# Performance work log

Hardware: AMD Instinct MI355X
Metric: run time of the kernel (lower is better)

Reference implementation:

```python
import jax, jax.numpy as jnp
import numpy as np

N_NODES = 50000
N_EDGES = 800000
IN_CH, HID_CH, OUT_CH = 128, 128, 64


def setup_inputs() -> dict:
    key = jax.random.key(0)
    k1, k2, k3, k4 = jax.random.split(key, 4)
    x = jax.random.normal(k1, (N_NODES, IN_CH), dtype=jnp.float32)
    edge_index = jax.random.randint(k2, (2, N_EDGES), 0, N_NODES, dtype=jnp.int64)
    # Glorot-style scaled weights (as in PyG GCNConv default init)
    W1 = jax.random.normal(k3, (IN_CH, HID_CH), dtype=jnp.float32) * (1.0 / np.sqrt(IN_CH))
    b1 = jnp.zeros((HID_CH,), dtype=jnp.float32)
    W2 = jax.random.normal(k4, (HID_CH, OUT_CH), dtype=jnp.float32) * (1.0 / np.sqrt(HID_CH))
    b2 = jnp.zeros((OUT_CH,), dtype=jnp.float32)
    return {"x": x, "edge_index": edge_index, "W1": W1, "b1": b1, "W2": W2, "b2": b2}


def _gcn_conv(x, src, dst, norm, W, b, n_nodes):
    # linear transform, then normalized gather-scatter aggregation
    h = x @ W                                   # [N, C_out]
    msgs = h[src] * norm[:, None]               # [E+N, C_out]
    agg = jax.ops.segment_sum(msgs, dst, num_segments=n_nodes)
    return agg + b


def reference(x, edge_index, W1, b1, W2, b2):
    n = x.shape[0]
    # add self-loops (PyG GCNConv default)
    loops = jnp.arange(n, dtype=edge_index.dtype)
    src = jnp.concatenate([edge_index[0], loops])  # message source (x_j)
    dst = jnp.concatenate([edge_index[1], loops])  # aggregation target
    # symmetric normalization: deg computed over targets incl. self-loops
    deg = jax.ops.segment_sum(jnp.ones_like(dst, dtype=x.dtype), dst, num_segments=n)
    dinv = jnp.where(deg > 0, jax.lax.rsqrt(deg), 0.0)
    norm = dinv[src] * dinv[dst]                # [E+N]

    h = _gcn_conv(x, src, dst, norm, W1, b1, n)
    h = jax.nn.relu(h)
    out = _gcn_conv(h, src, dst, norm, W2, b2, n)
    return out
```

## Files before the change

### kernel.cpp

```cpp
#include <hip/hip_runtime.h>
#include <hip/hip_bf16.h>


#define NPB 196
#define NBMAX 1024
#define CAP 4096

using short8 = __attribute__((ext_vector_type(8))) short;
using f32x4  = __attribute__((ext_vector_type(4))) float;

__device__ __forceinline__ unsigned short f2bf(float f) {
    unsigned int u = __float_as_uint(f);
    unsigned int r = u + 0x7fffu + ((u >> 16) & 1u);
    return (unsigned short)(r >> 16);
}

__global__ void k_zerob(int* __restrict__ p, int n) {
    int i = blockIdx.x * blockDim.x + threadIdx.x;
    if (i < n) p[i] = 0;
}

__global__ __launch_bounds__(256) void k_bhist(const int* __restrict__ dst,
                                               int* __restrict__ bhist,
                                               int nb, int e) {
    __shared__ int hist[NBMAX];
    const int tid = threadIdx.x;
    for (int b = tid; b < nb; b += 256) hist[b] = 0;
    __syncthreads();
    for (int i = blockIdx.x * 256 + tid; i < e; i += gridDim.x * 256)
        atomicAdd(&hist[dst[i] / NPB], 1);
    __syncthreads();
    for (int b = tid; b < nb; b += 256)
        if (hist[b]) atomicAdd(&bhist[b], hist[b]);
}

__global__ __launch_bounds__(64) void k_bscan(const int* __restrict__ bhist,
                                              int* __restrict__ bbase,
                                              int* __restrict__ bcursor,
                                              int nb, int e) {
    const int lane = threadIdx.x;
    int carry = 0;
    for (int base = 0; base < nb; base += 64) {
        int i = base + lane;
        int v = (i < nb) ? bhist[i] : 0;
        int s = v;
#pragma unroll
        for (int d = 1; d < 64; d <<= 1) {
            int u = __shfl_up(s, d);
            if (lane >= d) s += u;
        }
        int excl = carry + s - v;
        if (i < nb) { bbase[i] = excl; bcursor[i] = excl; }
        carry += __shfl(s, 63);
    }
    if (lane == 0) bbase[nb] = e;
}

__global__ __launch_bounds__(256) void k_bpart(const int* __restrict__ src,
                                               const int* __restrict__ dst,
                                               int* __restrict__ bcursor,
                                               int2* __restrict__ part,
                                               int nb, int e, int cpb) {
    __shared__ int chist[NBMAX];
    __shared__ int cbase[NBMAX];
    const int tid = threadIdx.x;
    const int e0 = blockIdx.x * cpb;
    const int e1 = min(e, e0 + cpb);
    for (int b = tid; b < nb; b += 256) chist[b] = 0;
    __syncthreads();
    for (int i = e0 + tid; i < e1; i += 256)
        atomicAdd(&chist[dst[i] / NPB], 1);
    __syncthreads();
    for (int b = tid; b < nb; b += 256) {
        int c = chist[b];
        cbase[b] = c ? atomicAdd(&bcursor[b], c) : 0;
        chist[b] = 0;
    }
    __syncthreads();
    for (int i = e0 + tid; i < e1; i += 256) {
        int d = dst[i];
        int bkt = d / NPB;
        int l = atomicAdd(&chist[bkt], 1);
        part[cbase[bkt] + l] = make_int2(src[i], d);
    }
}

__global__ __launch_bounds__(256) void k_bcsr(const int2* __restrict__ part,
                                              const int* __restrict__ bbase,
                                              int* __restrict__ offs,
                                              float* __restrict__ dinv,
                                              int* __restrict__ srcs,
                                              int n, int e) {
    __shared__ int cntL[256];
    __shared__ int srcsL[CAP];
    const int b = blockIdx.x;
    const int tid = threadIdx.x;
    const int eb0 = bbase[b], eb1 = bbase[b + 1];
    const int cnt = eb1 - eb0;
    const int n0 = b * NPB;
    const int npb = min(NPB, n - n0);

    if (tid < 256) cntL[tid] = 0;
    __syncthreads();
    for (int i = eb0 + tid; i < eb1; i += 256)
        atomicAdd(&cntL[part[i].y - n0], 1);
    __syncthreads();

    if (tid < 64) {
        const int lane = tid;
        int carry = 0;
        for (int base = 0; base < npb; base += 64) {
            int i = base + lane;
            int v = (i < npb) ? cntL[i] : 0;
            int s = v;
#pragma unroll
            for (int d = 1; d < 64; d <<= 1) {
                int u = __shfl_up(s, d);
                if (lane >= d) s += u;
            }
            int excl = carry + s - v;
            if (i < npb) {
                offs[n0 + i] = eb0 + excl;
                dinv[n0 + i] = rsqrtf((float)(v + 1));
                cntL[i] = excl;
            }
            carry += __shfl(s, 63);
        }
    }
    if (b == gridDim.x - 1 && tid == 0) offs[n] = e;
    __syncthreads();

    if (cnt <= CAP) {
        for (int i = eb0 + tid; i < eb1; i += 256) {
            int2 pr = part[i];
            int pos = atomicAdd(&cntL[pr.y - n0], 1);
            srcsL[pos] = pr.x;
        }
        __syncthreads();
        for (int i = tid; i < cnt; i += 256)
            srcs[eb0 + i] = srcsL[i];
    } else {
        for (int i = eb0 + tid; i < eb1; i += 256) {
            int2 pr = part[i];
            int pos = atomicAdd(&cntL[pr.y - n0], 1);
            srcs[eb0 + pos] = pr.x;
        }
    }
}

template <bool SRC_BF16>
__global__ __launch_bounds__(256) void k_gemm(const void* __restrict__ A,
                                              const float* __restrict__ W,
                                              const float* __restrict__ dinv,
                                              unsigned short* __restrict__ Cout,
                                              int M, int Ntot) {
    __shared__ __align__(16) unsigned short As_b[64][136];
    __shared__ __align__(16) unsigned short Bs_b[64][136];

    const int tid = threadIdx.x;
    const int bm = blockIdx.x * 64;
    const int bn = blockIdx.y * 64;

#pragma unroll
    for (int t = 0; t < 8; ++t) {
        int idx = tid + t * 256;
        int row = idx >> 5;
        int c4 = idx & 31;
        int gr = bm + row;
        ushort4 o = make_ushort4(0, 0, 0, 0);
        if (SRC_BF16) {
            if (gr < M)
                o = *(const ushort4*)&((const unsigned short*)A)[(size_t)gr * 128 + c4 * 4];
        } else {
            if (gr < M) {
                float4 f = *(const float4*)&((const float*)A)[(size_t)gr * 128 + c4 * 4];
                o = make_ushort4(f2bf(f.x), f2bf(f.y), f2bf(f.z), f2bf(f.w));
            }
        }
        *(ushort4*)&As_b[row][c4 * 4] = o;
    }

#pragma unroll
    for (int t = 0; t < 2; ++t) {
        int idx = tid + t * 256;
        int kb = idx >> 4;
        int c4 = idx & 15;
        int k0 = kb * 4;
        float4 f0 = *(const float4*)&W[(size_t)(k0 + 0) * Ntot + bn + c4 * 4];
        float4 f1 = *(const float4*)&W[(size_t)(k0 + 1) * Ntot + bn + c4 * 4];
        float4 f2 = *(const float4*)&W[(size_t)(k0 + 2) * Ntot + bn + c4 * 4];
        float4 f3 = *(const float4*)&W[(size_t)(k0 + 3) * Ntot + bn + c4 * 4];
        *(ushort4*)&Bs_b[c4 * 4 + 0][k0] =
            make_ushort4(f2bf(f0.x), f2bf(f1.x), f2bf(f2.x), f2bf(f3.x));
        *(ushort4*)&Bs_b[c4 * 4 + 1][k0] =
            make_ushort4(f2bf(f0.y), f2bf(f1.y), f2bf(f2.y), f2bf(f3.y));
        *(ushort4*)&Bs_b[c4 * 4 + 2][k0] =
            make_ushort4(f2bf(f0.z), f2bf(f1.z), f2bf(f2.z), f2bf(f3.z));
        *(ushort4*)&Bs_b[c4 * 4 + 3][k0] =
            make_ushort4(f2bf(f0.w), f2bf(f1.w), f2bf(f2.w), f2bf(f3.w));
    }
    __syncthreads();

    const int w = tid >> 6;
    const int l = tid & 63;
    const int wr = (w >> 1) * 32;
    const int wc = (w & 1) * 32;
    const int fr = l & 15;
    const int fk = (l >> 4) * 8;

    f32x4 acc[2][2] = {};

#pragma unroll
    for (int ks = 0; ks < 4; ++ks) {
        const int kof = ks * 32 + fk;
        short8 a0 = *(const short8*)&As_b[wr + fr][kof];
        short8 a1 = *(const short8*)&As_b[wr + 16 + fr][kof];
        short8 b0 = *(const short8*)&Bs_b[wc + fr][kof];
        short8 b1 = *(const short8*)&Bs_b[wc + 16 + fr][kof];
        acc[0][0] = __builtin_amdgcn_mfma_f32_16x16x32_bf16(a0, b0, acc[0][0], 0, 0, 0);
        acc[0][1] = __builtin_amdgcn_mfma_f32_16x16x32_bf16(a0, b1, acc[0][1], 0, 0, 0);
        acc[1][0] = __builtin_amdgcn_mfma_f32_16x16x32_bf16(a1, b0, acc[1][0], 0, 0, 0);
        acc[1][1] = __builtin_amdgcn_mfma_f32_16x16x32_bf16(a1, b1, acc[1][1], 0, 0, 0);
    }

#pragma unroll
    for (int i = 0; i < 2; ++i) {
#pragma unroll
        for (int r = 0; r < 4; ++r) {
            int gr = bm + wr + i * 16 + ((l >> 4) << 2) + r;
            if (gr < M) {
                float s = dinv[gr];
#pragma unroll
                for (int j = 0; j < 2; ++j) {
                    int gc = bn + wc + j * 16 + (l & 15);
                    Cout[(size_t)gr * Ntot + gc] = f2bf(acc[i][j][r] * s);
                }
            }
        }
    }
}

template <int C, bool OBF>
__global__ __launch_bounds__(256) void k_aggr(const unsigned short* __restrict__ hs,
                                              const int* __restrict__ srcs,
                                              const int* __restrict__ offs,
                                              const float* __restrict__ dinv,
                                              const float* __restrict__ bias,
                                              void* __restrict__ outp, int n) {
    constexpr int ROWB = C * 2;
    constexpr int LPE  = ROWB / 16;
    constexpr int EPL  = 64 / LPE;
    constexpr int CHUNK = 16;
    __shared__ __align__(1024) char smem[4][CHUNK * ROWB];

    const int lane = threadIdx.x & 63;
    const int wid  = threadIdx.x >> 6;
    const int node = blockIdx.x * 4 + wid;
    if (node >= n) return;
    char* region = smem[wid];

    float2 acc = make_float2(0.f, 0.f);

    const int off = offs[node], end = offs[node + 1];
    for (int base = off; base < end; base += 64) {
        const int m = end - base;
        int p = 0;
        if (lane < m) p = srcs[base + lane];
        const int cnt = m < 64 ? m : 64;

        for (int j0 = 0; j0 < cnt; j0 += CHUNK) {
            const int cc = min(CHUNK, cnt - j0);
            const int nload = (cc + EPL - 1) / EPL;
            for (int l = 0; l < nload; ++l) {
                int e = j0 + l * EPL + (lane / LPE);
                int srow = __shfl(p, e);
                const char* ga = (const char*)hs + (size_t)srow * ROWB + (lane % LPE) * 16;
                __builtin_amdgcn_global_load_lds(
                    (const __attribute__((address_space(1))) unsigned int*)ga,
                    (__attribute__((address_space(3))) unsigned int*)(region + l * 1024),
                    16, 0, 0);
            }
            asm volatile("s_waitcnt vmcnt(0)" ::: "memory");
            __builtin_amdgcn_sched_barrier(0);

            if (C == 128) {
                for (int j = 0; j < cc; ++j) {
                    unsigned int u = *(const unsigned int*)(region + j * ROWB + lane * 4);
                    acc.x += __uint_as_float(u << 16);
                    acc.y += __uint_as_float(u & 0xffff0000u);
                }
            } else {
                const int half = lane >> 5;
                const int rounds = (cc + 1) >> 1;
                for (int r = 0; r < rounds; ++r) {
                    int e = r * 2 + half;
                    unsigned int u = *(const unsigned int*)(region + e * ROWB + (lane & 31) * 4);
                    if (e >= cc) u = 0u;
                    acc.x += __uint_as_float(u << 16);
                    acc.y += __uint_as_float(u & 0xffff0000u);
                }
            }
        }
    }

    if (C == 64) {
        acc.x += __shfl_xor(acc.x, 32);
        acc.y += __shfl_xor(acc.y, 32);
        if (lane >= 32) return;
    }
    {
        unsigned int u = *(const unsigned int*)((const char*)hs + (size_t)node * ROWB + lane * 4);
        acc.x += __uint_as_float(u << 16);
        acc.y += __uint_as_float(u & 0xffff0000u);
        float di = dinv[node];
        float2 bb = *(const float2*)&bias[lane * 2];
        float vx = fmaf(acc.x, di, bb.x);
        float vy = fmaf(acc.y, di, bb.y);
        if (OBF) {
            unsigned short* ob = (unsigned short*)outp;
            ushort2 o = make_ushort2(f2bf(fmaxf(vx, 0.f)), f2bf(fmaxf(vy, 0.f)));
            *(ushort2*)&ob[(size_t)node * C + lane * 2] = o;
        } else {
            *(float2*)&((float*)outp)[(size_t)node * C + lane * 2] = make_float2(vx, vy);
        }
    }
}

extern "C" void kernel_launch(void* const* d_in, const int* in_sizes, int n_in,
                              void* d_out, int out_size, void* d_ws, size_t ws_size,
                              hipStream_t stream) {
    const float* x  = (const float*)d_in[0];
    const int*   ei = (const int*)d_in[1];
    const float* W1 = (const float*)d_in[2];
    const float* b1 = (const float*)d_in[3];
    const float* W2 = (const float*)d_in[4];
    const float* b2 = (const float*)d_in[5];
    float* out = (float*)d_out;

    const int N = in_sizes[0] / 128;
    const int E = in_sizes[1] / 2;
    const int* src = ei;
    const int* dst = ei + E;
    const int NB = (N + NPB - 1) / NPB;
    const int CPB = (E + 255) / 256;

    char* wsb = (char*)d_ws;
    size_t o = 0;
    auto alloc = [&](size_t bytes, size_t align) {
        o = (o + align - 1) & ~(align - 1);
        char* p = wsb + o;
        o += bytes;
        return p;
    };
    int*   bhist  = (int*)alloc((size_t)NB * 4, 4);
    int*   bbase  = (int*)alloc((size_t)(NB + 1) * 4, 4);
    int*   bcur   = (int*)alloc((size_t)NB * 4, 4);
    int2*  part   = (int2*)alloc((size_t)E * 8, 8);
    int*   offs   = (int*)alloc((size_t)(N + 1) * 4, 4);
    float* dinv   = (float*)alloc((size_t)N * 4, 4);
    int*   srcs   = (int*)alloc((size_t)E * 4, 4);
    unsigned short* hs1   = (unsigned short*)alloc((size_t)N * 128 * 2, 16);
    unsigned short* hs2   = (unsigned short*)alloc((size_t)N * 64 * 2, 16);
    unsigned short* agg1b = (unsigned short*)alloc((size_t)N * 128 * 2, 16);

    k_zerob<<<1, 1024, 0, stream>>>(bhist, NB);
    k_bhist<<<256, 256, 0, stream>>>(dst, bhist, NB, E);
    k_bscan<<<1, 64, 0, stream>>>(bhist, bbase, bcur, NB, E);
    k_bpart<<<256, 256, 0, stream>>>(src, dst, bcur, part, NB, E, CPB);
    k_bcsr<<<NB, 256, 0, stream>>>(part, bbase, offs, dinv, srcs, N, E);

    const int gm = (N + 63) / 64;
    const int ga = (N + 3) / 4;

    k_gemm<false><<<dim3(gm, 2), 256, 0, stream>>>(x, W1, dinv, hs1, N, 128);
    k_aggr<128, true><<<ga, 256, 0, stream>>>(hs1, srcs, offs, dinv, b1, agg1b, N);

    k_gemm<true><<<dim3(gm, 1), 256, 0, stream>>>(agg1b, W2, dinv, hs2, N, 64);
    k_aggr<64, false><<<ga, 256, 0, stream>>>(hs2, srcs, offs, dinv, b2, out, N);
}
```

Before: 136.3 us.

## Fold self-loops into CSR and balance aggregation by edge ranges per wave

The CSR build now inserts each node's self-loop as an explicit edge, which removes the special-case self term in aggregation. The aggregation kernels no longer assign one wave per node. Each wave takes a contiguous slice of the combined edge list, finds its node range by binary search on the offsets, and streams 32-row gathers through LDS, finalizing each node when its edge range ends. This targets load imbalance and the underused lanes on low-degree nodes. It costs extra index work per edge, binary searches, and serial per-node finalize branches inside the inner loop.

Result: slower. 167.6 us (+22.9%).

```diff
diff --git a/kernel.cpp b/kernel.cpp
--- a/kernel.cpp
+++ b/kernel.cpp
@@ -90,7 +90,7 @@
                                               int* __restrict__ offs,
                                               float* __restrict__ dinv,
                                               int* __restrict__ srcs,
-                                              int n, int e) {
+                                              int n, int etot) {
     __shared__ int cntL[256];
     __shared__ int srcsL[CAP];
     const int b = blockIdx.x;
@@ -99,6 +99,9 @@
     const int cnt = eb1 - eb0;
     const int n0 = b * NPB;
     const int npb = min(NPB, n - n0);
+    const int out0 = eb0 + b * NPB;
+    const int total = cnt + npb;
+    const bool lds_path = (total <= CAP);
 
     if (tid < 256) cntL[tid] = 0;
     __syncthreads();
@@ -111,7 +114,7 @@
         int carry = 0;
         for (int base = 0; base < npb; base += 64) {
             int i = base + lane;
-            int v = (i < npb) ? cntL[i] : 0;
+            int v = (i < npb) ? cntL[i] + 1 : 0;
             int s = v;
 #pragma unroll
             for (int d = 1; d < 64; d <<= 1) {
@@ -120,30 +123,32 @@
             }
             int excl = carry + s - v;
             if (i < npb) {
-                offs[n0 + i] = eb0 + excl;
-                dinv[n0 + i] = rsqrtf((float)(v + 1));
-                cntL[i] = excl;
+                offs[n0 + i] = out0 + excl;
+                dinv[n0 + i] = rsqrtf((float)v);
+                if (lds_path) srcsL[excl] = n0 + i;
+                else          srcs[out0 + excl] = n0 + i;
+                cntL[i] = excl + 1;
             }
             carry += __shfl(s, 63);
         }
     }
-    if (b == gridDim.x - 1 && tid == 0) offs[n] = e;
-    __syncthreads();
-
-    if (cnt <= CAP) {
+    if (b == gridDim.x - 1 && tid == 0) offs[n] = etot;
+    __syncthreads();
+
+    if (lds_path) {
         for (int i = eb0 + tid; i < eb1; i += 256) {
             int2 pr = part[i];
             int pos = atomicAdd(&cntL[pr.y - n0], 1);
             srcsL[pos] = pr.x;
         }
         __syncthreads();
-        for (int i = tid; i < cnt; i += 256)
-            srcs[eb0 + i] = srcsL[i];
+        for (int i = tid; i < total; i += 256)
+            srcs[out0 + i] = srcsL[i];
     } else {
         for (int i = eb0 + tid; i < eb1; i += 256) {
             int2 pr = part[i];
             int pos = atomicAdd(&cntL[pr.y - n0], 1);
-            srcs[eb0 + pos] = pr.x;
+            srcs[out0 + pos] = pr.x;
         }
     }
 }
@@ -246,84 +251,109 @@
                                               const int* __restrict__ offs,
                                               const float* __restrict__ dinv,
                                               const float* __restrict__ bias,
-                                              void* __restrict__ outp, int n) {
+                                              void* __restrict__ outp,
+                                              int n, int etot, int epw, int nw) {
     constexpr int ROWB = C * 2;
     constexpr int LPE  = ROWB / 16;
     constexpr int EPL  = 64 / LPE;
-    constexpr int CHUNK = 16;
-    __shared__ __align__(1024) char smem[4][CHUNK * ROWB];
+    constexpr int RGB  = 32 * ROWB;
+    __shared__ __align__(1024) char smem[4][RGB];
 
     const int lane = threadIdx.x & 63;
     const int wid  = threadIdx.x >> 6;
-    const int node = blockIdx.x * 4 + wid;
-    if (node >= n) return;
-    char* region = smem[wid];
-
+    const int w = blockIdx.x * 4 + wid;
+    if (w >= nw) return;
+    char* R = smem[wid];
+
+    const int lo = w * epw;
+    if (lo >= etot) return;
+    const int hi = (w == nw - 1) ? etot + 1 : lo + epw;
+
+    auto lb = [&](int target) {
+        int l = 0, h = n + 1;
+        while (l < h) { int m = (l + h) >> 1; if (offs[m] >= target) h = m; else l = m + 1; }
+        return l;
+    };
+    int nstart = lb(lo);
+    int nend = lb(hi); if (nend > n) nend = n;
+    if (nstart >= nend) return;
+    const int ebeg = offs[nstart], eend = offs[nend];
+
+    int mbase = nstart;
+    int offs_l = offs[(mbase + lane) <= n ? (mbase + lane) : n];
+    float dinv_l = dinv[(mbase + lane) < n ? (mbase + lane) : (n - 1)];
+    int cur = nstart;
+    int next_end = __shfl(offs_l, cur + 1 - mbase);
+
+    float2 bb;
+    if (C == 128) bb = *(const float2*)&bias[lane * 2];
+    else          bb = *(const float2*)&bias[(lane & 31) * 2];
     float2 acc = make_float2(0.f, 0.f);
 
-    const int off = offs[node], end = offs[node + 1];
-    for (int base = off; base < end; base += 64) {
-        const int m = end - base;
-        int p = 0;
-        if (lane < m) p = srcs[base + lane];
-        const int cnt = m < 64 ? m : 64;
-
-        for (int j0 = 0; j0 < cnt; j0 += CHUNK) {
-            const int cc = min(CHUNK, cnt - j0);
-            const int nload = (cc + EPL - 1) / EPL;
-            for (int l = 0; l < nload; ++l) {
-                int e = j0 + l * EPL + (lane / LPE);
+    auto finalize = [&]() {
+        float di = __shfl(dinv_l, cur - mbase);
+        float vx = fmaf(acc.x, di, bb.x);
+        float vy = fmaf(acc.y, di, bb.y);
+        if (C == 128) {
+            if (OBF) {
+                ushort2 o = make_ushort2(f2bf(fmaxf(vx, 0.f)), f2bf(fmaxf(vy, 0.f)));
+                *(ushort2*)&((unsigned short*)outp)[(size_t)cur * C + lane * 2] = o;
+            } else {
+                *(float2*)&((float*)outp)[(size_t)cur * C + lane * 2] = make_float2(vx, vy);
+            }
+        } else {
+            if (lane < 32) {
+                if (OBF) {
+                    ushort2 o = make_ushort2(f2bf(fmaxf(vx, 0.f)), f2bf(fmaxf(vy, 0.f)));
+                    *(ushort2*)&((unsigned short*)outp)[(size_t)cur * C + lane * 2] = o;
+                } else {
+                    *(float2*)&((float*)outp)[(size_t)cur * C + lane * 2] = make_float2(vx, vy);
+                }
+            }
+        }
+        acc = make_float2(0.f, 0.f);
+    };
+
+    for (int dwb = ebeg; dwb < eend; dwb += 64) {
+        int p = (dwb + lane < eend) ? srcs[dwb + lane] : 0;
+#pragma unroll
+        for (int h2 = 0; h2 < 2; ++h2) {
+            const int base = dwb + h2 * 32;
+            if (base >= eend) break;
+            int cnt = eend - base; if (cnt > 32) cnt = 32;
+            const int nload = (cnt + EPL - 1) / EPL;
+            for (int g = 0; g < nload; ++g) {
+                int e = h2 * 32 + g * EPL + (lane / LPE);
                 int srow = __shfl(p, e);
                 const char* ga = (const char*)hs + (size_t)srow * ROWB + (lane % LPE) * 16;
                 __builtin_amdgcn_global_load_lds(
                     (const __attribute__((address_space(1))) unsigned int*)ga,
-                    (__attribute__((address_space(3))) unsigned int*)(region + l * 1024),
+                    (__attribute__((address_space(3))) unsigned int*)(R + g * 1024),
                     16, 0, 0);
             }
             asm volatile("s_waitcnt vmcnt(0)" ::: "memory");
             __builtin_amdgcn_sched_barrier(0);
 
-            if (C == 128) {
-                for (int j = 0; j < cc; ++j) {
-                    unsigned int u = *(const unsigned int*)(region + j * ROWB + lane * 4);
-                    acc.x += __uint_as_float(u << 16);
-                    acc.y += __uint_as_float(u & 0xffff0000u);
+            for (int j = 0; j < cnt; ++j) {
+                int eidx = base + j;
+                while (eidx == next_end) {
+                    finalize();
+                    ++cur;
+                    if (cur + 1 - mbase > 63) {
+                        mbase = cur;
+                        offs_l = offs[(mbase + lane) <= n ? (mbase + lane) : n];
+                        dinv_l = dinv[(mbase + lane) < n ? (mbase + lane) : (n - 1)];
+                    }
+                    next_end = __shfl(offs_l, cur + 1 - mbase);
                 }
-            } else {
-                const int half = lane >> 5;
-                const int rounds = (cc + 1) >> 1;
-                for (int r = 0; r < rounds; ++r) {
-                    int e = r * 2 + half;
-                    unsigned int u = *(const unsigned int*)(region + e * ROWB + (lane & 31) * 4);
-                    if (e >= cc) u = 0u;
-                    acc.x += __uint_as_float(u << 16);
-                    acc.y += __uint_as_float(u & 0xffff0000u);
-                }
-            }
-        }
-    }
-
-    if (C == 64) {
-        acc.x += __shfl_xor(acc.x, 32);
-        acc.y += __shfl_xor(acc.y, 32);
-        if (lane >= 32) return;
-    }
-    {
-        unsigned int u = *(const unsigned int*)((const char*)hs + (size_t)node * ROWB + lane * 4);
-        acc.x += __uint_as_float(u << 16);
-        acc.y += __uint_as_float(u & 0xffff0000u);
-        float di = dinv[node];
-        float2 bb = *(const float2*)&bias[lane * 2];
-        float vx = fmaf(acc.x, di, bb.x);
-        float vy = fmaf(acc.y, di, bb.y);
-        if (OBF) {
-            unsigned short* ob = (unsigned short*)outp;
-            ushort2 o = make_ushort2(f2bf(fmaxf(vx, 0.f)), f2bf(fmaxf(vy, 0.f)));
-            *(ushort2*)&ob[(size_t)node * C + lane * 2] = o;
-        } else {
-            *(float2*)&((float*)outp)[(size_t)node * C + lane * 2] = make_float2(vx, vy);
-        }
-    }
+                unsigned int u = *(const unsigned int*)(
+                    R + j * ROWB + ((C == 128) ? lane * 4 : (lane & 31) * 4));
+                acc.x += __uint_as_float(u << 16);
+                acc.y += __uint_as_float(u & 0xffff0000u);
+            }
+        }
+    }
+    finalize();
 }
 
 extern "C" void kernel_launch(void* const* d_in, const int* in_sizes, int n_in,
@@ -343,6 +373,7 @@
     const int* dst = ei + E;
     const int NB = (N + NPB - 1) / NPB;
     const int CPB = (E + 255) / 256;
+    const int ET = E + N;
 
     char* wsb = (char*)d_ws;
     size_t o = 0;
@@ -358,7 +389,7 @@
     int2*  part   = (int2*)alloc((size_t)E * 8, 8);
     int*   offs   = (int*)alloc((size_t)(N + 1) * 4, 4);
     float* dinv   = (float*)alloc((size_t)N * 4, 4);
-    int*   srcs   = (int*)alloc((size_t)E * 4, 4);
+    int*   srcs   = (int*)alloc((size_t)ET * 4, 4);
     unsigned short* hs1   = (unsigned short*)alloc((size_t)N * 128 * 2, 16);
     unsigned short* hs2   = (unsigned short*)alloc((size_t)N * 64 * 2, 16);
     unsigned short* agg1b = (unsigned short*)alloc((size_t)N * 128 * 2, 16);
@@ -367,14 +398,20 @@
     k_bhist<<<256, 256, 0, stream>>>(dst, bhist, NB, E);
     k_bscan<<<1, 64, 0, stream>>>(bhist, bbase, bcur, NB, E);
     k_bpart<<<256, 256, 0, stream>>>(src, dst, bcur, part, NB, E, CPB);
-    k_bcsr<<<NB, 256, 0, stream>>>(part, bbase, offs, dinv, srcs, N, E);
+    k_bcsr<<<NB, 256, 0, stream>>>(part, bbase, offs, dinv, srcs, N, ET);
 
     const int gm = (N + 63) / 64;
-    const int ga = (N + 3) / 4;
+
+    const int NW1 = 5120, BL1 = NW1 / 4;
+    const int EPW1 = (ET + NW1 - 1) / NW1;
+    const int NW2 = 8192, BL2 = NW2 / 4;
+    const int EPW2 = (ET + NW2 - 1) / NW2;
 
     k_gemm<false><<<dim3(gm, 2), 256, 0, stream>>>(x, W1, dinv, hs1, N, 128);
-    k_aggr<128, true><<<ga, 256, 0, stream>>>(hs1, srcs, offs, dinv, b1, agg1b, N);
+    k_aggr<128, true><<<BL1, 256, 0, stream>>>(hs1, srcs, offs, dinv, b1, agg1b,
+                                               N, ET, EPW1, NW1);
 
     k_gemm<true><<<dim3(gm, 1), 256, 0, stream>>>(agg1b, W2, dinv, hs2, N, 64);
-    k_aggr<64, false><<<ga, 256, 0, stream>>>(hs2, srcs, offs, dinv, b2, out, N);
-}
+    k_aggr<64, false><<<BL2, 256, 0, stream>>>(hs2, srcs, offs, dinv, b2, out,
+                                               N, ET, EPW2, NW2);
+}
```
